# Performance work log

Measured on AMD Instinct MI355X. Metric: run time of the kernel, lower is better.

Reference implementation:

```python
import jax, jax.numpy as jnp
import numpy as np

EMBED_DIM = 768
NUM_HEAD = 12
HEAD_DIM = 64
SCALE = 1.0 / np.sqrt(HEAD_DIM)


def setup_inputs() -> dict:
    key = jax.random.key(0)
    k1, k2, k3, k4 = jax.random.split(key, 4)
    B, T = 2, 2048
    x = jax.random.normal(k1, (B, T, EMBED_DIM), dtype=jnp.float32)
    # nn.Linear(embed_dim, 3*embed_dim, bias=True): weight [3E, E], bias [3E]
    w_qkv = jax.random.normal(k2, (3 * EMBED_DIM, EMBED_DIM), dtype=jnp.float32) * (1.0 / np.sqrt(EMBED_DIM))
    b_qkv = jax.random.normal(k3, (3 * EMBED_DIM,), dtype=jnp.float32) * 0.02
    # nn.Linear(embed_dim, embed_dim, bias=False): weight [E, E]
    w_final = jax.random.normal(k4, (EMBED_DIM, EMBED_DIM), dtype=jnp.float32) * (1.0 / np.sqrt(EMBED_DIM))
    return {"x": x, "w_qkv": w_qkv, "b_qkv": b_qkv, "w_final": w_final}


def reference(x, w_qkv, b_qkv, w_final):
    B, T, E = x.shape
    # qkv projection: x @ W^T + b  -> [B, T, 3E]
    qkv = jnp.einsum('bte,fe->btf', x, w_qkv) + b_qkv
    q, k, v = jnp.split(qkv, 3, axis=-1)

    def heads(t):  # [B, T, E] -> [B, H, T, D]
        return t.reshape(B, T, NUM_HEAD, HEAD_DIM).transpose(0, 2, 1, 3)

    q, k, v = heads(q), heads(k), heads(v)
    # scores [B, H, T, T]
    scores = jnp.einsum('bhtd,bhsd->bhts', q, k) * SCALE
    causal = jnp.tril(jnp.ones((T, T), dtype=bool))
    scores = jnp.where(causal, scores, -jnp.inf)
    attn = jax.nn.softmax(scores, axis=-1)  # dropout off (eval mode)
    out = jnp.einsum('bhts,bhsd->bhtd', attn, v)  # [B, H, T, D]
    out = out.transpose(0, 2, 1, 3).reshape(B, T, NUM_HEAD * HEAD_DIM)
    return jnp.einsum('bte,fe->btf', out, w_final)
```

## Files before the change

kernel.cpp:

```cpp
#include <hip/hip_runtime.h>
#include <cstdint>

typedef _Float16 f16x8 __attribute__((ext_vector_type(8)));
typedef _Float16 f16x4 __attribute__((ext_vector_type(4)));
typedef float    f32x4 __attribute__((ext_vector_type(4)));

static constexpr int TB = 2;
static constexpr int TT = 2048;
static constexpr int TE = 768;
static constexpr int TH = 12;
static constexpr int TD = 64;
static constexpr int TM = TB * TT;
static constexpr int TK = TE;
static constexpr int NQKV = 3 * TE;

#define SCALE_LOG2E 0.18033688011112042f

__device__ __forceinline__ void gload16(const void* g, void* lds) {
  __builtin_amdgcn_global_load_lds(
      (__attribute__((address_space(1))) void*)(uintptr_t)g,
      (__attribute__((address_space(3))) void*)(uint32_t)(uintptr_t)lds, 16, 0, 0);
}

__global__ void cvt3(const float* __restrict__ x, const float* __restrict__ wq,
                     const float* __restrict__ wf, _Float16* __restrict__ xh,
                     _Float16* __restrict__ wqh, _Float16* __restrict__ wfh) {
  const int NX = TM * TK / 4, NW = NQKV * TK / 4;
  int i = blockIdx.x * 256 + threadIdx.x;
  if (i < NX) {
    float4 v = ((const float4*)x)[i];
    f16x4 o = {(_Float16)v.x, (_Float16)v.y, (_Float16)v.z, (_Float16)v.w};
    *(f16x4*)&xh[(size_t)i * 4] = o;
  } else {
    const float4* src; _Float16* dst; int j;
    if (i < NX + NW) { src = (const float4*)wq; dst = wqh; j = i - NX; }
    else             { src = (const float4*)wf; dst = wfh; j = i - NX - NW; }
    float4 v = src[j];
    f16x4 o = {(_Float16)v.x, (_Float16)v.y, (_Float16)v.z, (_Float16)v.w};
    const int flat = j * 4;
    const int n = flat / TK, k = flat % TK;
    const size_t idx = ((size_t)(n >> 4) * 24 + (k >> 5)) * 512 +
                       ((k >> 3) & 3) * 128 + (n & 15) * 8 + (k & 7);
    *(f16x4*)&dst[idx] = o;
  }
}

template <int EPI, int MT, int NXT, int MPX>
__global__ __launch_bounds__(MT * 4)
void gemm_nt(const _Float16* __restrict__ A, const _Float16* __restrict__ Bw,
             const float* __restrict__ bias,
             _Float16* __restrict__ qb, _Float16* __restrict__ kb,
             _Float16* __restrict__ vtb, float* __restrict__ outp) {
  __shared__ _Float16 As[3][MT * 64];
  const int tid = threadIdx.x;
  const int w = tid >> 6, lane = tid & 63;
  const int lr = lane & 15, lk = lane >> 4;

  const int id = blockIdx.x;
  const int xcd = id & 7, j = id >> 3;
  const int m0 = (xcd * MPX + j / NXT) * MT;
  const int n0 = (j % NXT) * 128;
  const int wr = (MT == 128) ? (w >> 2) : 0;
  const int wc = (MT == 128) ? (w & 3) : w;

  f32x4 acc[4][2] = {};
  const char* Ab = (const char*)(A + (size_t)m0 * TK);
  const char* WB = (const char*)Bw;
  const int nb = (n0 >> 4) + wc * 2;
  constexpr int NS = TK / 64;

  auto loadB = [&](int ks, f16x8 (&bf)[2][2]) {
#pragma unroll
    for (int ni = 0; ni < 2; ++ni)
#pragma unroll
      for (int kc = 0; kc < 2; ++kc)
        bf[ni][kc] = *(const f16x8*)(WB +
                                     ((size_t)(nb + ni) * 24 + ks * 2 + kc) * 1024 +
                                     lane * 16);
  };
  auto stageA = [&](int ks, _Float16* L) {
#pragma unroll
    for (int c = 0; c < 2; ++c) {
      int g = w * 2 + c;
      int o = g * 1024 + lane * 16;
      int row = o >> 7, ch = (o >> 4) & 7;
      gload16(Ab + (size_t)row * (TK * 2) + ks * 128 + ((ch ^ (row & 7)) << 4),
              (char*)L + g * 1024);
    }
  };
  auto step = [&](f16x8 (&bc)[2][2], f16x8 (&bn)[2][2], _Float16* Lc,
                  _Float16* Ln, int ks) {
    if (ks < NS - 1) {
      asm volatile("s_waitcnt vmcnt(6)" ::: "memory");
    } else {
      asm volatile("s_waitcnt vmcnt(0)" ::: "memory");
    }
    __builtin_amdgcn_s_barrier();
    if (ks < NS - 2) {
      loadB(ks + 2, bn);
      stageA(ks + 2, Ln);
    }
#pragma unroll
    for (int kc = 0; kc < 2; ++kc) {
      f16x8 af[4];
#pragma unroll
      for (int mi = 0; mi < 4; ++mi) {
        int row = wr * 64 + mi * 16 + lr;
        af[mi] = *(const f16x8*)&Lc[row * 64 + (((kc * 4 + lk) ^ (row & 7)) << 3)];
      }
#pragma unroll
      for (int mi = 0; mi < 4; ++mi)
#pragma unroll
        for (int ni = 0; ni < 2; ++ni)
          acc[mi][ni] = __builtin_amdgcn_mfma_f32_16x16x32_f16(af[mi], bc[ni][kc],
                                                               acc[mi][ni], 0, 0, 0);
    }
  };

  f16x8 b0[2][2], b1[2][2], b2[2][2];
  loadB(0, b0);
  stageA(0, As[0]);
  loadB(1, b1);
  stageA(1, As[1]);
  for (int kss = 0; kss < NS; kss += 3) {
    step(b0, b2, As[0], As[2], kss);
    step(b1, b0, As[1], As[0], kss + 1);
    step(b2, b1, As[2], As[1], kss + 2);
  }

#pragma unroll
  for (int mi = 0; mi < 4; ++mi) {
#pragma unroll
    for (int ni = 0; ni < 2; ++ni) {
      const int col = n0 + wc * 32 + ni * 16 + lr;
#pragma unroll
      for (int r = 0; r < 4; ++r) {
        const int row = m0 + wr * 64 + mi * 16 + lk * 4 + r;
        float v = acc[mi][ni][r];
        if (EPI == 0) {
          v += bias[col];
          const int which = (col >= 2 * TE) ? 2 : (col >= TE ? 1 : 0);
          const int e = col - which * TE;
          const int h = e >> 6, d = e & 63;
          const int b = row >> 11, t = row & (TT - 1);
          const size_t hb = (size_t)(b * TH + h);
          if (which == 0) {
            qb[(hb * TT + t) * TD + d] = (_Float16)(v * SCALE_LOG2E);
          } else if (which == 1) {
            kb[((((hb * 128 + (t >> 4)) * 8 + (d >> 3)) * 16 + (t & 15)) * 8) +
               (d & 7)] = (_Float16)v;
          } else {
            const int kc = (t >> 5) & 1, hi = (t >> 4) & 1;
            const int lkv = (t >> 2) & 3, m = t & 3;
            vtb[((((((hb * 32 + (t >> 6)) * 4 + (d >> 4)) * 2 + kc) * 4 + lkv) *
                      16 +
                  (d & 15)) *
                 8) +
                (hi * 4 + m)] = (_Float16)v;
          }
        } else {
          outp[(size_t)row * TE + col] = v;
        }
      }
    }
  }
}

__global__ __launch_bounds__(256)
void attn_kernel(const _Float16* __restrict__ qbuf, const _Float16* __restrict__ kbuf,
                 const _Float16* __restrict__ vtbuf, _Float16* __restrict__ ob) {
  const int tid = threadIdx.x, w = tid >> 6, lane = tid & 63;
  const int lr = lane & 15, lk = lane >> 4;

  const int id = blockIdx.x;
  const int bh = id % 24;
  const int qt = 31 - id / 24;
  const int t0 = qt * 64;
  const int nt = qt + 1, ntm1 = qt;

  const _Float16* q = qbuf + (size_t)bh * (TT * TD);
  const char* kbase =
      (const char*)(kbuf + (size_t)bh * (TT * TD)) + lk * 256 + lr * 16;
  const char* vbase =
      (const char*)(vtbuf + (size_t)bh * (TT * TD)) + lk * 256 + lr * 16;

  f16x8 qf[2];
#pragma unroll
  for (int kc = 0; kc < 2; ++kc)
    qf[kc] = *(const f16x8*)&q[(size_t)(t0 + w * 16 + lr) * TD + kc * 32 + lk * 8];

  f32x4 of[4] = {};
  float mrun = -1e30f, lrun = 0.f;

  f16x8 kfA[2][4], kfB[2][4], vf[2][4];

#pragma unroll
  for (int kc = 0; kc < 2; ++kc)
#pragma unroll
    for (int ni = 0; ni < 4; ++ni)
      kfA[kc][ni] = *(const f16x8*)(kbase + ni * 2048 + kc * 1024);
  {
    const char* k1 = kbase + (size_t)(nt > 1 ? 1 : 0) * 8192;
#pragma unroll
    for (int kc = 0; kc < 2; ++kc)
#pragma unroll
      for (int ni = 0; ni < 4; ++ni)
        kfB[kc][ni] = *(const f16x8*)(k1 + ni * 2048 + kc * 1024);
  }

  auto phase = [&](f16x8 (&kf)[2][4], int st) {
    const char* vt = vbase + (size_t)st * 8192;
#pragma unroll
    for (int kc = 0; kc < 2; ++kc)
#pragma unroll
      for (int nd = 0; nd < 4; ++nd)
        vf[kc][nd] = *(const f16x8*)(vt + nd * 2048 + kc * 1024);

    f32x4 sa[4] = {};
    __builtin_amdgcn_s_setprio(1);
#pragma unroll
    for (int kc = 0; kc < 2; ++kc)
#pragma unroll
      for (int ni = 0; ni < 4; ++ni)
        sa[ni] =
            __builtin_amdgcn_mfma_f32_16x16x32_f16(kf[kc][ni], qf[kc], sa[ni], 0, 0, 0);
    __builtin_amdgcn_s_setprio(0);

    {
      const int stp = (st + 2 <= ntm1) ? st + 2 : ntm1;
      const char* kt = kbase + (size_t)stp * 8192;
#pragma unroll
      for (int kc = 0; kc < 2; ++kc)
#pragma unroll
        for (int ni = 0; ni < 4; ++ni)
          kf[kc][ni] = *(const f16x8*)(kt + ni * 2048 + kc * 1024);
    }

    if (st == ntm1) {
      const int s0 = st * 64;
#pragma unroll
      for (int ni = 0; ni < 4; ++ni)
#pragma unroll
        for (int r = 0; r < 4; ++r)
          if (s0 + ni * 16 + lk * 4 + r > t0 + w * 16 + lr) sa[ni][r] = -1e30f;
    }

    float mx;
    {
      float m0_ = fmaxf(fmaxf(sa[0][0], sa[0][1]), fmaxf(sa[0][2], sa[0][3]));
      float m1_ = fmaxf(fmaxf(sa[1][0], sa[1][1]), fmaxf(sa[1][2], sa[1][3]));
      float m2_ = fmaxf(fmaxf(sa[2][0], sa[2][1]), fmaxf(sa[2][2], sa[2][3]));
      float m3_ = fmaxf(fmaxf(sa[3][0], sa[3][1]), fmaxf(sa[3][2], sa[3][3]));
      mx = fmaxf(fmaxf(m0_, m1_), fmaxf(m2_, m3_));
      mx = fmaxf(mx, __shfl_xor(mx, 16));
      mx = fmaxf(mx, __shfl_xor(mx, 32));
    }

    if (__any(mx > mrun + 8.0f)) {
      float mn = fmaxf(mrun, mx);
      float al = __builtin_amdgcn_exp2f(mrun - mn);
      mrun = mn;
      lrun *= al;
      float al4[4];
#pragma unroll
      for (int r = 0; r < 4; ++r) al4[r] = __shfl(al, lk * 4 + r);
#pragma unroll
      for (int nd = 0; nd < 4; ++nd)
#pragma unroll
        for (int r = 0; r < 4; ++r) of[nd][r] *= al4[r];
    }

    f16x8 pa[2];
    float rs;
    {
      float rn[4];
#pragma unroll
      for (int ni = 0; ni < 4; ++ni) {
        float p0 = __builtin_amdgcn_exp2f(sa[ni][0] - mrun);
        float p1 = __builtin_amdgcn_exp2f(sa[ni][1] - mrun);
        float p2 = __builtin_amdgcn_exp2f(sa[ni][2] - mrun);
        float p3 = __builtin_amdgcn_exp2f(sa[ni][3] - mrun);
        rn[ni] = (p0 + p1) + (p2 + p3);
        pa[ni >> 1][(ni & 1) * 4 + 0] = (_Float16)p0;
        pa[ni >> 1][(ni & 1) * 4 + 1] = (_Float16)p1;
        pa[ni >> 1][(ni & 1) * 4 + 2] = (_Float16)p2;
        pa[ni >> 1][(ni & 1) * 4 + 3] = (_Float16)p3;
      }
      rs = (rn[0] + rn[1]) + (rn[2] + rn[3]);
      rs += __shfl_xor(rs, 16);
      rs += __shfl_xor(rs, 32);
    }
    lrun += rs;

    __builtin_amdgcn_s_setprio(1);
#pragma unroll
    for (int kc = 0; kc < 2; ++kc)
#pragma unroll
      for (int nd = 0; nd < 4; ++nd)
        of[nd] =
            __builtin_amdgcn_mfma_f32_16x16x32_f16(pa[kc], vf[kc][nd], of[nd], 0, 0, 0);
    __builtin_amdgcn_s_setprio(0);
  };

  int st = 0;
  while (st + 1 < nt) {
    phase(kfA, st);
    phase(kfB, st + 1);
    st += 2;
  }
  if (st < nt) phase(kfA, st);

  float linv[4];
#pragma unroll
  for (int r = 0; r < 4; ++r) linv[r] = __shfl(lrun, lk * 4 + r);
  const int b = bh / TH, h = bh - b * TH;
#pragma unroll
  for (int nd = 0; nd < 4; ++nd) {
#pragma unroll
    for (int r = 0; r < 4; ++r) {
      int tg = t0 + w * 16 + lk * 4 + r;
      int d = nd * 16 + lr;
      ob[(size_t)(b * TT + tg) * TE + h * TD + d] = (_Float16)(of[nd][r] / linv[r]);
    }
  }
}

extern "C" void kernel_launch(void* const* d_in, const int* in_sizes, int n_in,
                              void* d_out, int out_size, void* d_ws, size_t ws_size,
                              hipStream_t stream) {
  const float* x    = (const float*)d_in[0];
  const float* wqkv = (const float*)d_in[1];
  const float* bqkv = (const float*)d_in[2];
  const float* wfin = (const float*)d_in[3];
  float* out = (float*)d_out;

  _Float16* xh  = (_Float16*)d_ws;
  _Float16* wqh = xh + (size_t)TM * TK;
  _Float16* wfh = wqh + (size_t)NQKV * TK;
  _Float16* qb  = wfh + (size_t)TE * TE;
  _Float16* kb  = qb + (size_t)TM * TE;
  _Float16* vtb = kb + (size_t)TM * TE;
  _Float16* ob  = vtb + (size_t)TM * TE;

  cvt3<<<5376, 256, 0, stream>>>(x, wqkv, wfin, xh, wqh, wfh);
  gemm_nt<0, 64, NQKV / 128, 8><<<8 * 8 * (NQKV / 128), 256, 0, stream>>>(
      xh, wqh, bqkv, qb, kb, vtb, nullptr);
  attn_kernel<<<dim3(TT / 64 * TB * TH), 256, 0, stream>>>(qb, kb, vtb, ob);
  gemm_nt<1, 64, TE / 128, 8><<<8 * 8 * (TE / 128), 256, 0, stream>>>(
      ob, wfh, nullptr, nullptr, nullptr, nullptr, out);
}
```

Measured before the change: 82.18 us.

## Split long causal query tiles across two blocks and merge partial softmax results

After: 86.14 us. 4.8% more time.

```diff
diff --git a/kernel.cpp b/kernel.cpp
--- a/kernel.cpp
+++ b/kernel.cpp
@@ -168,15 +168,32 @@
 
 __global__ __launch_bounds__(256)
 void attn_kernel(const _Float16* __restrict__ qbuf, const _Float16* __restrict__ kbuf,
-                 const _Float16* __restrict__ vtbuf, _Float16* __restrict__ ob) {
+                 const _Float16* __restrict__ vtbuf, _Float16* __restrict__ ob,
+                 float* __restrict__ pm, float* __restrict__ pl,
+                 _Float16* __restrict__ po) {
   const int tid = threadIdx.x, w = tid >> 6, lane = tid & 63;
   const int lr = lane & 15, lk = lane >> 4;
 
   const int id = blockIdx.x;
   const int bh = id % 24;
-  const int qt = 31 - id / 24;
+  const int slot = id / 24;
+  int qt, sBeg, sEnd, part, heavy;
+  if (slot < 32) {
+    heavy = 1;
+    qt = 31 - (slot >> 1);
+    part = slot & 1;
+    const int half = (qt + 2) >> 1;
+    sBeg = part ? half : 0;
+    sEnd = part ? qt + 1 : half;
+  } else {
+    heavy = 0;
+    qt = 47 - slot;
+    part = 0;
+    sBeg = 0;
+    sEnd = qt + 1;
+  }
   const int t0 = qt * 64;
-  const int nt = qt + 1, ntm1 = qt;
+  const int last = sEnd - 1;
 
   const _Float16* q = qbuf + (size_t)bh * (TT * TD);
   const char* kbase =
@@ -194,18 +211,16 @@
 
   f16x8 kfA[2][4], kfB[2][4], vf[2][4];
 
-#pragma unroll
-  for (int kc = 0; kc < 2; ++kc)
-#pragma unroll
-    for (int ni = 0; ni < 4; ++ni)
-      kfA[kc][ni] = *(const f16x8*)(kbase + ni * 2048 + kc * 1024);
   {
-    const char* k1 = kbase + (size_t)(nt > 1 ? 1 : 0) * 8192;
+    const char* k0 = kbase + (size_t)sBeg * 8192;
+    const char* k1 = kbase + (size_t)((sBeg + 1 <= last) ? sBeg + 1 : last) * 8192;
 #pragma unroll
     for (int kc = 0; kc < 2; ++kc)
 #pragma unroll
-      for (int ni = 0; ni < 4; ++ni)
+      for (int ni = 0; ni < 4; ++ni) {
+        kfA[kc][ni] = *(const f16x8*)(k0 + ni * 2048 + kc * 1024);
         kfB[kc][ni] = *(const f16x8*)(k1 + ni * 2048 + kc * 1024);
+      }
   }
 
   auto phase = [&](f16x8 (&kf)[2][4], int st) {
@@ -227,7 +242,7 @@
     __builtin_amdgcn_s_setprio(0);
 
     {
-      const int stp = (st + 2 <= ntm1) ? st + 2 : ntm1;
+      const int stp = (st + 2 <= last) ? st + 2 : last;
       const char* kt = kbase + (size_t)stp * 8192;
 #pragma unroll
       for (int kc = 0; kc < 2; ++kc)
@@ -236,7 +251,7 @@
           kf[kc][ni] = *(const f16x8*)(kt + ni * 2048 + kc * 1024);
     }
 
-    if (st == ntm1) {
+    if (st == qt) {
       const int s0 = st * 64;
 #pragma unroll
       for (int ni = 0; ni < 4; ++ni)
@@ -302,27 +317,72 @@
     __builtin_amdgcn_s_setprio(0);
   };
 
-  int st = 0;
-  while (st + 1 < nt) {
+  int st = sBeg;
+  while (st + 1 < sEnd) {
     phase(kfA, st);
     phase(kfB, st + 1);
     st += 2;
   }
-  if (st < nt) phase(kfA, st);
+  if (st < sEnd) phase(kfA, st);
 
   float linv[4];
 #pragma unroll
   for (int r = 0; r < 4; ++r) linv[r] = __shfl(lrun, lk * 4 + r);
+
+  if (!heavy) {
+    const int b = bh / TH, h = bh - b * TH;
+#pragma unroll
+    for (int nd = 0; nd < 4; ++nd)
+#pragma unroll
+      for (int r = 0; r < 4; ++r) {
+        int tg = t0 + w * 16 + lk * 4 + r;
+        int d = nd * 16 + lr;
+        ob[(size_t)(b * TT + tg) * TE + h * TD + d] =
+            (_Float16)(of[nd][r] / linv[r]);
+      }
+  } else {
+    const int u = (bh * 16 + (qt - 16)) * 2 + part;
+    if (lk == 0) {
+      pm[u * 64 + w * 16 + lr] = mrun;
+      pl[u * 64 + w * 16 + lr] = lrun;
+    }
+#pragma unroll
+    for (int nd = 0; nd < 4; ++nd)
+#pragma unroll
+      for (int r = 0; r < 4; ++r) {
+        int row = w * 16 + lk * 4 + r;
+        int d = nd * 16 + lr;
+        po[(size_t)u * 4096 + row * 64 + d] = (_Float16)(of[nd][r] / linv[r]);
+      }
+  }
+}
+
+__global__ __launch_bounds__(256)
+void merge_kernel(const float* __restrict__ pm, const float* __restrict__ pl,
+                  const _Float16* __restrict__ po, _Float16* __restrict__ ob) {
+  const int bh = blockIdx.x % 24, qidx = blockIdx.x / 24;
+  const int qt = 16 + qidx;
+  const int u0 = (bh * 16 + qidx) * 2, u1 = u0 + 1;
+  const int row = threadIdx.x >> 2;
+  const int d0 = (threadIdx.x & 3) * 16;
+
+  const float m0 = pm[u0 * 64 + row], m1 = pm[u1 * 64 + row];
+  const float l0 = pl[u0 * 64 + row], l1 = pl[u1 * 64 + row];
+  const float mm = fmaxf(m0, m1);
+  float w0 = __builtin_amdgcn_exp2f(m0 - mm) * l0;
+  float w1 = __builtin_amdgcn_exp2f(m1 - mm) * l1;
+  const float rden = 1.0f / (w0 + w1);
+  w0 *= rden;
+  w1 *= rden;
+
   const int b = bh / TH, h = bh - b * TH;
-#pragma unroll
-  for (int nd = 0; nd < 4; ++nd) {
-#pragma unroll
-    for (int r = 0; r < 4; ++r) {
-      int tg = t0 + w * 16 + lk * 4 + r;
-      int d = nd * 16 + lr;
-      ob[(size_t)(b * TT + tg) * TE + h * TD + d] = (_Float16)(of[nd][r] / linv[r]);
-    }
-  }
+  const int tg = qt * 64 + row;
+  const _Float16* o0 = po + (size_t)u0 * 4096 + row * 64 + d0;
+  const _Float16* o1 = po + (size_t)u1 * 4096 + row * 64 + d0;
+  _Float16* dst = ob + (size_t)(b * TT + tg) * TE + h * TD + d0;
+#pragma unroll
+  for (int j = 0; j < 16; ++j)
+    dst[j] = (_Float16)(w0 * (float)o0[j] + w1 * (float)o1[j]);
 }
 
 extern "C" void kernel_launch(void* const* d_in, const int* in_sizes, int n_in,
@@ -341,11 +401,15 @@
   _Float16* kb  = qb + (size_t)TM * TE;
   _Float16* vtb = kb + (size_t)TM * TE;
   _Float16* ob  = vtb + (size_t)TM * TE;
+  _Float16* po  = ob + (size_t)TM * TE;
+  float* pm = (float*)(po + (size_t)768 * 4096);
+  float* pl = pm + 768 * 64;
 
   cvt3<<<5376, 256, 0, stream>>>(x, wqkv, wfin, xh, wqh, wfh);
   gemm_nt<0, 64, NQKV / 128, 8><<<8 * 8 * (NQKV / 128), 256, 0, stream>>>(
       xh, wqh, bqkv, qb, kb, vtb, nullptr);
-  attn_kernel<<<dim3(TT / 64 * TB * TH), 256, 0, stream>>>(qb, kb, vtb, ob);
+  attn_kernel<<<24 * 48, 256, 0, stream>>>(qb, kb, vtb, ob, pm, pl, po);
+  merge_kernel<<<24 * 16, 256, 0, stream>>>(pm, pl, po, ob);
   gemm_nt<1, 64, TE / 128, 8><<<8 * 8 * (TE / 128), 256, 0, stream>>>(
       ob, wfh, nullptr, nullptr, nullptr, nullptr, out);
 }
```

## Stage K/V tiles through triple-buffered LDS with async global-to-LDS loads

Applied to the files above, without the earlier changes.

Result: slower. 85.74 us (+4.3%).

```diff
diff --git a/kernel.cpp b/kernel.cpp
--- a/kernel.cpp
+++ b/kernel.cpp
@@ -169,6 +169,7 @@
 __global__ __launch_bounds__(256)
 void attn_kernel(const _Float16* __restrict__ qbuf, const _Float16* __restrict__ kbuf,
                  const _Float16* __restrict__ vtbuf, _Float16* __restrict__ ob) {
+  __shared__ _Float16 KV[3][8192];
   const int tid = threadIdx.x, w = tid >> 6, lane = tid & 63;
   const int lr = lane & 15, lk = lane >> 4;
 
@@ -176,13 +177,22 @@
   const int bh = id % 24;
   const int qt = 31 - id / 24;
   const int t0 = qt * 64;
-  const int nt = qt + 1, ntm1 = qt;
+  const int nt = qt + 1;
 
   const _Float16* q = qbuf + (size_t)bh * (TT * TD);
-  const char* kbase =
-      (const char*)(kbuf + (size_t)bh * (TT * TD)) + lk * 256 + lr * 16;
-  const char* vbase =
-      (const char*)(vtbuf + (size_t)bh * (TT * TD)) + lk * 256 + lr * 16;
+  const char* kg = (const char*)(kbuf + (size_t)bh * (TT * TD));
+  const char* vg = (const char*)(vtbuf + (size_t)bh * (TT * TD));
+
+  auto stage = [&](int st, int buf) {
+    char* Lb = (char*)KV[buf];
+    const char* base = (w < 2) ? kg : vg;
+#pragma unroll
+    for (int c4 = 0; c4 < 4; ++c4) {
+      const int cl = (w & 1) * 4 + c4;
+      gload16(base + (size_t)st * 8192 + cl * 1024 + lane * 16,
+              Lb + ((w < 2) ? 0 : 8192) + cl * 1024);
+    }
+  };
 
   f16x8 qf[2];
 #pragma unroll
@@ -192,29 +202,36 @@
   f32x4 of[4] = {};
   float mrun = -1e30f, lrun = 0.f;
 
-  f16x8 kfA[2][4], kfB[2][4], vf[2][4];
-
-#pragma unroll
-  for (int kc = 0; kc < 2; ++kc)
-#pragma unroll
-    for (int ni = 0; ni < 4; ++ni)
-      kfA[kc][ni] = *(const f16x8*)(kbase + ni * 2048 + kc * 1024);
-  {
-    const char* k1 = kbase + (size_t)(nt > 1 ? 1 : 0) * 8192;
+  stage(0, 0);
+  stage((nt > 1) ? 1 : 0, 1);
+
+  int cur = 0;
+  for (int st = 0; st < nt; ++st) {
+    if (st < nt - 1) {
+      asm volatile("s_waitcnt vmcnt(4)" ::: "memory");
+    } else {
+      asm volatile("s_waitcnt vmcnt(0)" ::: "memory");
+    }
+    __builtin_amdgcn_s_barrier();
+    if (st + 2 < nt) {
+      int b2 = cur + 2;
+      if (b2 >= 3) b2 -= 3;
+      stage(st + 2, b2);
+    }
+
+    const char* Lb = (const char*)KV[cur];
+    f16x8 kf[2][4], vf[2][4];
 #pragma unroll
     for (int kc = 0; kc < 2; ++kc)
 #pragma unroll
       for (int ni = 0; ni < 4; ++ni)
-        kfB[kc][ni] = *(const f16x8*)(k1 + ni * 2048 + kc * 1024);
-  }
-
-  auto phase = [&](f16x8 (&kf)[2][4], int st) {
-    const char* vt = vbase + (size_t)st * 8192;
+        kf[kc][ni] = *(const f16x8*)(Lb + ni * 2048 + kc * 1024 + lane * 16);
 #pragma unroll
     for (int kc = 0; kc < 2; ++kc)
 #pragma unroll
       for (int nd = 0; nd < 4; ++nd)
-        vf[kc][nd] = *(const f16x8*)(vt + nd * 2048 + kc * 1024);
+        vf[kc][nd] =
+            *(const f16x8*)(Lb + 8192 + nd * 2048 + kc * 1024 + lane * 16);
 
     f32x4 sa[4] = {};
     __builtin_amdgcn_s_setprio(1);
@@ -226,17 +243,7 @@
             __builtin_amdgcn_mfma_f32_16x16x32_f16(kf[kc][ni], qf[kc], sa[ni], 0, 0, 0);
     __builtin_amdgcn_s_setprio(0);
 
-    {
-      const int stp = (st + 2 <= ntm1) ? st + 2 : ntm1;
-      const char* kt = kbase + (size_t)stp * 8192;
-#pragma unroll
-      for (int kc = 0; kc < 2; ++kc)
-#pragma unroll
-        for (int ni = 0; ni < 4; ++ni)
-          kf[kc][ni] = *(const f16x8*)(kt + ni * 2048 + kc * 1024);
-    }
-
-    if (st == ntm1) {
+    if (st == nt - 1) {
       const int s0 = st * 64;
 #pragma unroll
       for (int ni = 0; ni < 4; ++ni)
@@ -300,15 +307,9 @@
         of[nd] =
             __builtin_amdgcn_mfma_f32_16x16x32_f16(pa[kc], vf[kc][nd], of[nd], 0, 0, 0);
     __builtin_amdgcn_s_setprio(0);
-  };
-
-  int st = 0;
-  while (st + 1 < nt) {
-    phase(kfA, st);
-    phase(kfB, st + 1);
-    st += 2;
-  }
-  if (st < nt) phase(kfA, st);
+
+    cur = (cur + 1 == 3) ? 0 : cur + 1;
+  }
 
   float linv[4];
 #pragma unroll
```
